# Kernel optimization log

Measured on AMD Instinct MI355X. Metric: run time of the kernel, lower is better.

## Reference

```python
import jax, jax.numpy as jnp
import numpy as np

EPS = 1e-7  # keras backend.epsilon()
NUM_ROUTING = 3


def squash(v, axis=-1):
    s2 = jnp.sum(jnp.square(v), axis=axis, keepdims=True)
    scale = s2 / (1.0 + s2) / jnp.sqrt(s2 + EPS)
    return scale * v


def setup_inputs() -> dict:
    key = jax.random.key(0)
    k1, k2 = jax.random.split(key)
    B, I, Q = 64, 2048, 16      # batch, input_num_capsule, input_dim_capsule
    J, P = 32, 32               # num_capsule, dim_capsule
    inputs = jax.random.normal(k1, (B, I, Q), dtype=jnp.float32)
    # glorot-ish scale for W: [num_capsule, input_num_capsule, dim_capsule, input_dim_capsule]
    W = jax.random.normal(k2, (J, I, P, Q), dtype=jnp.float32) * (1.0 / np.sqrt(Q))
    return {"inputs": inputs, "W": W}


def reference(inputs, W):
    # inputs_hat[b,j,i,p] = sum_q inputs[b,i,q] * W[j,i,p,q]
    hat = jnp.einsum('biq,jipq->bjip', inputs, W)
    hat_stop = jax.lax.stop_gradient(hat)
    B, J, I, P = hat.shape
    b = jnp.zeros((B, J, I), dtype=hat.dtype)
    for _ in range(NUM_ROUTING - 1):
        c = jax.nn.softmax(b, axis=1)                       # softmax over num_capsule axis
        v = squash(jnp.einsum('bji,bjip->bjp', c, hat_stop))
        b = b + jnp.einsum('bjp,bjip->bji', v, hat_stop)
    c = jax.nn.softmax(b, axis=1)
    return squash(jnp.einsum('bji,bjip->bjp', c, hat))      # [B, J, P]
```

## Files before the change

kernel.cpp:

```cpp
#include <hip/hip_runtime.h>

typedef _Float16 h8 __attribute__((ext_vector_type(8)));
typedef _Float16 h4 __attribute__((ext_vector_type(4)));
typedef float f4 __attribute__((ext_vector_type(4)));

constexpr int NB = 64;
constexpr int NI = 2048;
constexpr int NQ = 16;
constexpr int NJ = 32;
constexpr int NP = 32;
constexpr int NIP = NI / 2;
constexpr int VSZ = NB * NJ * NP;


__global__ __launch_bounds__(256)
void zero_kernel(f4* __restrict__ p)
{
    const f4 z = {0.f, 0.f, 0.f, 0.f};
    p[(size_t)blockIdx.x * 256 + threadIdx.x] = z;
}

__global__ __launch_bounds__(256)
void xpack_kernel(const float* __restrict__ X, h8* __restrict__ xp)
{
    const int ip = blockIdx.x;
    const int t = threadIdx.x;
    const int bf = t >> 6, l = t & 63;
    const int b = (l & 15) + 16 * bf;
    const int i = 2 * ip + (l >= 32 ? 1 : 0);
    const int q0 = ((l >> 4) & 1) * 8;
    const float* xs = X + ((size_t)b * NI + i) * NQ + q0;
    const float4 u = *reinterpret_cast<const float4*>(xs);
    const float4 v = *reinterpret_cast<const float4*>(xs + 4);
    h8 h;
    h[0] = (_Float16)u.x; h[1] = (_Float16)u.y; h[2] = (_Float16)u.z; h[3] = (_Float16)u.w;
    h[4] = (_Float16)v.x; h[5] = (_Float16)v.y; h[6] = (_Float16)v.z; h[7] = (_Float16)v.w;
    xp[(size_t)(ip * 4 + bf) * 64 + l] = h;
}

__device__ inline float sqscale(float s2)
{
    return s2 / ((1.f + s2) * sqrtf(s2 + 1e-7f));
}

__global__ __launch_bounds__(512)
void wacc_kernel(const float* __restrict__ Wg, const h8* __restrict__ xp,
                 h8* __restrict__ wp, float* __restrict__ ACC)
{
    const int t = threadIdx.x, wv = t >> 6, l = t & 63;
    const int j = blockIdx.x >> 4, is = blockIdx.x & 15;
    const int ioff = (l >= 32) ? 1 : 0;
    const int q0 = ((l >> 4) & 1) * 8;
    const int pbase = is * 64 + wv * 8;

    f4 D[2][4];
#pragma unroll
    for (int pf = 0; pf < 2; ++pf)
#pragma unroll
        for (int bf = 0; bf < 4; ++bf) { f4 Z = {0.f, 0.f, 0.f, 0.f}; D[pf][bf] = Z; }

    const float* wgl = Wg + ((size_t)j * NI + ioff) * (NP * NQ) + (size_t)(l & 15) * NQ + q0;

    f4 u0, u1, v0, v1;
    {
        const float* s0 = wgl + (size_t)(2 * pbase) * (NP * NQ);
        u0 = *reinterpret_cast<const f4*>(s0);
        u1 = *reinterpret_cast<const f4*>(s0 + 4);
        v0 = *reinterpret_cast<const f4*>(s0 + 16 * NQ);
        v1 = *reinterpret_cast<const f4*>(s0 + 16 * NQ + 4);
    }
    h8 B0, B1, B2, B3;
    {
        const h8* xpb = xp + (size_t)pbase * 4 * 64 + l;
        B0 = xpb[0]; B1 = xpb[64]; B2 = xpb[128]; B3 = xpb[192];
    }

#pragma unroll 1
    for (int ipl = 0; ipl < 8; ++ipl) {
        const int ipg = pbase + ipl;
        const int nip = (ipl < 7) ? ipg + 1 : ipg;
        f4 nu0, nu1, nv0, nv1;
        {
            const float* s0 = wgl + (size_t)(2 * nip) * (NP * NQ);
            nu0 = *reinterpret_cast<const f4*>(s0);
            nu1 = *reinterpret_cast<const f4*>(s0 + 4);
            nv0 = *reinterpret_cast<const f4*>(s0 + 16 * NQ);
            nv1 = *reinterpret_cast<const f4*>(s0 + 16 * NQ + 4);
        }
        h8 nB0, nB1, nB2, nB3;
        {
            const h8* xpb = xp + (size_t)nip * 4 * 64 + l;
            nB0 = xpb[0]; nB1 = xpb[64]; nB2 = xpb[128]; nB3 = xpb[192];
        }

        h8 A0, A1;
#pragma unroll
        for (int e = 0; e < 4; ++e) {
            A0[e] = (_Float16)u0[e]; A0[e + 4] = (_Float16)u1[e];
            A1[e] = (_Float16)v0[e]; A1[e + 4] = (_Float16)v1[e];
        }
        const size_t wo = ((size_t)j * NIP + ipg) * 2 * 64 + l;
        wp[wo] = A0;
        wp[wo + 64] = A1;
        D[0][0] = __builtin_amdgcn_mfma_f32_16x16x32_f16(A0, B0, D[0][0], 0, 0, 0);
        D[1][0] = __builtin_amdgcn_mfma_f32_16x16x32_f16(A1, B0, D[1][0], 0, 0, 0);
        D[0][1] = __builtin_amdgcn_mfma_f32_16x16x32_f16(A0, B1, D[0][1], 0, 0, 0);
        D[1][1] = __builtin_amdgcn_mfma_f32_16x16x32_f16(A1, B1, D[1][1], 0, 0, 0);
        D[0][2] = __builtin_amdgcn_mfma_f32_16x16x32_f16(A0, B2, D[0][2], 0, 0, 0);
        D[1][2] = __builtin_amdgcn_mfma_f32_16x16x32_f16(A1, B2, D[1][2], 0, 0, 0);
        D[0][3] = __builtin_amdgcn_mfma_f32_16x16x32_f16(A0, B3, D[0][3], 0, 0, 0);
        D[1][3] = __builtin_amdgcn_mfma_f32_16x16x32_f16(A1, B3, D[1][3], 0, 0, 0);
        u0 = nu0; u1 = nu1; v0 = nv0; v1 = nv1;
        B0 = nB0; B1 = nB1; B2 = nB2; B3 = nB3;
    }

    __shared__ float R[8][64 * 36];
#pragma unroll
    for (int pf = 0; pf < 2; ++pf)
#pragma unroll
        for (int bf = 0; bf < 4; ++bf) {
            const int b = (l & 15) + 16 * bf, p = (l >> 4) * 4 + 16 * pf;
            *reinterpret_cast<f4*>(&R[wv][b * 36 + p]) = D[pf][bf];
        }
    __syncthreads();
#pragma unroll
    for (int k = 0; k < 4; ++k) {
        const int id = t + k * 512;
        const int b = id >> 5, p = id & 31;
        float s = 0.f;
#pragma unroll
        for (int w8 = 0; w8 < 8; ++w8) s += R[w8][b * 36 + p];
        atomicAdd(ACC + ((size_t)b * NJ + j) * NP + p, s);
    }
}

__global__ __launch_bounds__(512)
void logits_kernel(const h8* __restrict__ wp, const h8* __restrict__ xp,
                   const float* __restrict__ S, _Float16* __restrict__ cp)
{
    __shared__ float L[8][32][64];
    const int t = threadIdx.x, wv = t >> 6, l = t & 63;
    const int i0 = blockIdx.x * 8;
    const int ip0 = blockIdx.x * 4;
    const bool lo = l >= 32;
    h8 zh;
#pragma unroll
    for (int e = 0; e < 8; ++e) zh[e] = (_Float16)0.f;

#pragma unroll 1
    for (int jj = 0; jj < 4; ++jj) {
        const int j = wv * 4 + jj;

        float sreg[4][8];
#pragma unroll
        for (int bf = 0; bf < 4; ++bf) {
            const int b = (l & 15) + 16 * bf;
            const size_t base = ((size_t)b * NJ + j) * NP + (l >> 4) * 4;
            const f4 s0 = *reinterpret_cast<const f4*>(S + base);
            const f4 s1 = *reinterpret_cast<const f4*>(S + base + 16);
#pragma unroll
            for (int r = 0; r < 4; ++r) { sreg[bf][r] = s0[r]; sreg[bf][4 + r] = s1[r]; }
        }

        const h8* wj = wp + (size_t)j * NIP * 2 * 64 + l;
        h8 A0 = wj[(size_t)ip0 * 128];
        h8 A1 = wj[(size_t)ip0 * 128 + 64];

#pragma unroll 1
        for (int ipl = 0; ipl < 4; ++ipl) {
            const int ipg = ip0 + ipl;
            const int nip = (ipl < 3) ? ipg + 1 : ipg;
            h8 nA0 = wj[(size_t)nip * 128];
            h8 nA1 = wj[(size_t)nip * 128 + 64];

            const h8* xpb = xp + (size_t)ipg * 4 * 64 + l;

#pragma unroll
            for (int half = 0; half < 2; ++half) {
                f4 D[2][4];
#pragma unroll
                for (int pf = 0; pf < 2; ++pf)
#pragma unroll
                    for (int bf = 0; bf < 4; ++bf) { f4 Z = {0.f, 0.f, 0.f, 0.f}; D[pf][bf] = Z; }
#pragma unroll
                for (int bfp = 0; bfp < 2; ++bfp) {
                    const h8 Ba = xpb[(2 * bfp) * 64];
                    const h8 Bb = xpb[(2 * bfp + 1) * 64];
                    const h8 Bma = ((half == 0) == lo) ? zh : Ba;
                    const h8 Bmb = ((half == 0) == lo) ? zh : Bb;
                    D[0][2 * bfp]     = __builtin_amdgcn_mfma_f32_16x16x32_f16(A0, Bma, D[0][2 * bfp], 0, 0, 0);
                    D[1][2 * bfp]     = __builtin_amdgcn_mfma_f32_16x16x32_f16(A1, Bma, D[1][2 * bfp], 0, 0, 0);
                    D[0][2 * bfp + 1] = __builtin_amdgcn_mfma_f32_16x16x32_f16(A0, Bmb, D[0][2 * bfp + 1], 0, 0, 0);
                    D[1][2 * bfp + 1] = __builtin_amdgcn_mfma_f32_16x16x32_f16(A1, Bmb, D[1][2 * bfp + 1], 0, 0, 0);
                }
                float part[4];
#pragma unroll
                for (int bf = 0; bf < 4; ++bf) {
                    float p_ = 0.f;
#pragma unroll
                    for (int pf = 0; pf < 2; ++pf)
#pragma unroll
                        for (int r = 0; r < 4; ++r) p_ += sreg[bf][pf * 4 + r] * D[pf][bf][r];
                    p_ += __shfl_xor(p_, 16);
                    p_ += __shfl_xor(p_, 32);
                    part[bf] = p_;
                }
                const int hb = l >> 4;
                const float wval = hb == 0 ? part[0] : hb == 1 ? part[1] : hb == 2 ? part[2] : part[3];
                L[ipl * 2 + half][j][(l & 15) + 16 * hb] = wval;
            }
            A0 = nA0; A1 = nA1;
        }
    }
    __syncthreads();

    {
        const int b = t & 63, ii = t >> 6;
        float lv[32];
        float m = -1e30f;
#pragma unroll
        for (int j = 0; j < 32; ++j) { lv[j] = L[ii][j][b]; m = fmaxf(m, lv[j]); }
        float s = 0.f;
#pragma unroll
        for (int j = 0; j < 32; ++j) { lv[j] = __expf(lv[j] - m); s += lv[j]; }
        const float inv = 1.f / s;
#pragma unroll
        for (int j = 0; j < 32; ++j) L[ii][j][b] = lv[j] * inv;
    }
    __syncthreads();

    {
        const int jw = t >> 4, r = t & 15;
#pragma unroll 1
        for (int ii = 0; ii < 8; ++ii) {
            h4 c4;
#pragma unroll
            for (int e = 0; e < 4; ++e) c4[e] = (_Float16)L[ii][jw][16 * e + r];
            *reinterpret_cast<h4*>(cp + ((size_t)jw * NI + i0 + ii) * 64 + r * 4) = c4;
        }
    }
}

__global__ __launch_bounds__(512)
void accum_kernel(const h8* __restrict__ wp, const h8* __restrict__ xp,
                  const _Float16* __restrict__ cp, float* __restrict__ ACC)
{
    const int t = threadIdx.x, wv = t >> 6, l = t & 63;
    const int j = blockIdx.x >> 4, is = blockIdx.x & 15;
    const int ioff = (l >= 32) ? 1 : 0;

    f4 D[2][4];
#pragma unroll
    for (int pf = 0; pf < 2; ++pf)
#pragma unroll
        for (int bf = 0; bf < 4; ++bf) { f4 Z = {0.f, 0.f, 0.f, 0.f}; D[pf][bf] = Z; }

    const int pbase = is * 64 + wv * 8;
    const h8* wj = wp + (size_t)j * NIP * 2 * 64 + l;
    const _Float16* cj = cp + ((size_t)j * NI + ioff) * 64 + (l & 15) * 4;

    h8 A0 = wj[(size_t)pbase * 128];
    h8 A1 = wj[(size_t)pbase * 128 + 64];
    h8 B0, B1, B2, B3;
    {
        const h8* xpb = xp + (size_t)pbase * 4 * 64 + l;
        B0 = xpb[0]; B1 = xpb[64]; B2 = xpb[128]; B3 = xpb[192];
    }
    h4 c4 = *reinterpret_cast<const h4*>(cj + (size_t)(2 * pbase) * 64);

#pragma unroll 1
    for (int ipl = 0; ipl < 8; ++ipl) {
        const int ipg = pbase + ipl;
        const int nip = (ipl < 7) ? ipg + 1 : ipg;
        h8 nA0 = wj[(size_t)nip * 128];
        h8 nA1 = wj[(size_t)nip * 128 + 64];
        h8 nB0, nB1, nB2, nB3;
        {
            const h8* xpb = xp + (size_t)nip * 4 * 64 + l;
            nB0 = xpb[0]; nB1 = xpb[64]; nB2 = xpb[128]; nB3 = xpb[192];
        }
        h4 nc4 = *reinterpret_cast<const h4*>(cj + (size_t)(2 * nip) * 64);

        h8 b0 = B0 * c4[0], b1 = B1 * c4[1], b2 = B2 * c4[2], b3 = B3 * c4[3];
        D[0][0] = __builtin_amdgcn_mfma_f32_16x16x32_f16(A0, b0, D[0][0], 0, 0, 0);
        D[1][0] = __builtin_amdgcn_mfma_f32_16x16x32_f16(A1, b0, D[1][0], 0, 0, 0);
        D[0][1] = __builtin_amdgcn_mfma_f32_16x16x32_f16(A0, b1, D[0][1], 0, 0, 0);
        D[1][1] = __builtin_amdgcn_mfma_f32_16x16x32_f16(A1, b1, D[1][1], 0, 0, 0);
        D[0][2] = __builtin_amdgcn_mfma_f32_16x16x32_f16(A0, b2, D[0][2], 0, 0, 0);
        D[1][2] = __builtin_amdgcn_mfma_f32_16x16x32_f16(A1, b2, D[1][2], 0, 0, 0);
        D[0][3] = __builtin_amdgcn_mfma_f32_16x16x32_f16(A0, b3, D[0][3], 0, 0, 0);
        D[1][3] = __builtin_amdgcn_mfma_f32_16x16x32_f16(A1, b3, D[1][3], 0, 0, 0);
        A0 = nA0; A1 = nA1; B0 = nB0; B1 = nB1; B2 = nB2; B3 = nB3; c4 = nc4;
    }

    __shared__ float R[8][64 * 36];
#pragma unroll
    for (int pf = 0; pf < 2; ++pf)
#pragma unroll
        for (int bf = 0; bf < 4; ++bf) {
            const int b = (l & 15) + 16 * bf, p = (l >> 4) * 4 + 16 * pf;
            *reinterpret_cast<f4*>(&R[wv][b * 36 + p]) = D[pf][bf];
        }
    __syncthreads();
#pragma unroll
    for (int k = 0; k < 4; ++k) {
        const int id = t + k * 512;
        const int b = id >> 5, p = id & 31;
        float s = 0.f;
#pragma unroll
        for (int w8 = 0; w8 < 8; ++w8) s += R[w8][b * 36 + p];
        atomicAdd(ACC + ((size_t)b * NJ + j) * NP + p, s);
    }
}

__global__ __launch_bounds__(256)
void squash_kernel(const float* __restrict__ U, const float* __restrict__ ADD,
                   float* __restrict__ OUT, float scale)
{
    const int t   = threadIdx.x;
    const int row = blockIdx.x * 8 + (t >> 5);
    const int p   = t & 31;
    const float val = U[row * 32 + p] * scale;
    float sq = val * val;
#pragma unroll
    for (int d = 1; d < 32; d <<= 1) sq += __shfl_xor(sq, d);
    float o = val * sqscale(sq);
    if (ADD != nullptr) o += ADD[row * 32 + p];
    OUT[row * 32 + p] = o;
}

extern "C" void kernel_launch(void* const* d_in, const int* in_sizes, int n_in,
                              void* d_out, int out_size, void* d_ws, size_t ws_size,
                              hipStream_t stream)
{
    const float* X  = (const float*)d_in[0];
    const float* Wg = (const float*)d_in[1];
    float* out = (float*)d_out;

    float* v1u = (float*)d_ws;
    float* v2u = v1u + VSZ;
    float* ou  = v2u + VSZ;
    float* S2  = ou  + VSZ;
    float* S3  = S2  + VSZ;
    h8* xp = (h8*)((char*)d_ws + (size_t)5 * VSZ * 4);
    _Float16* cp = (_Float16*)((char*)xp + (size_t)NIP * 4 * 64 * 16);
    h8* wpk = (h8*)((char*)cp + (size_t)NJ * NI * 64 * 2);

    xpack_kernel<<<NIP, 256, 0, stream>>>(X, xp);
    zero_kernel<<<3 * VSZ * 4 / (256 * 16), 256, 0, stream>>>((f4*)d_ws);

    wacc_kernel<<<512, 512, 0, stream>>>(Wg, xp, wpk, v1u);

    squash_kernel<<<VSZ / 256, 256, 0, stream>>>(v1u, nullptr, S2, 1.f / 32.f);
    logits_kernel<<<NI / 8, 512, 0, stream>>>(wpk, xp, S2, cp);
    accum_kernel<<<512, 512, 0, stream>>>(wpk, xp, cp, v2u);

    squash_kernel<<<VSZ / 256, 256, 0, stream>>>(v2u, S2, S3, 1.f);
    logits_kernel<<<NI / 8, 512, 0, stream>>>(wpk, xp, S3, cp);
    accum_kernel<<<512, 512, 0, stream>>>(wpk, xp, cp, ou);

    squash_kernel<<<VSZ / 256, 256, 0, stream>>>(ou, nullptr, out, 1.f);
}
```

Measured before the change: 136.5 us.

## Process two output capsules per block in accum kernel, sharing input fragments

Each block of the accumulation kernel now handles a pair of j capsules over half as many i-pairs per wave. The packed input (B) fragments are loaded once and reused across both j's. The grid keeps the same block count, and the loop count per wave drops from 8 to 4. The explicit software prefetch of the next iteration's operands is removed and replaced by straight loads, and the LDS reduction is done twice, once per j. The change cuts x-fragment traffic but costs double the accumulator registers and may expose load latency without the prefetch.

```diff
diff --git a/kernel.cpp b/kernel.cpp
--- a/kernel.cpp
+++ b/kernel.cpp
@@ -246,70 +246,81 @@
                   const _Float16* __restrict__ cp, float* __restrict__ ACC)
 {
     const int t = threadIdx.x, wv = t >> 6, l = t & 63;
-    const int j = blockIdx.x >> 4, is = blockIdx.x & 15;
+    const int jp = blockIdx.x >> 5, is = blockIdx.x & 31;
+    const int j0 = jp * 2;
     const int ioff = (l >= 32) ? 1 : 0;
 
-    f4 D[2][4];
-#pragma unroll
-    for (int pf = 0; pf < 2; ++pf)
-#pragma unroll
-        for (int bf = 0; bf < 4; ++bf) { f4 Z = {0.f, 0.f, 0.f, 0.f}; D[pf][bf] = Z; }
-
-    const int pbase = is * 64 + wv * 8;
-    const h8* wj = wp + (size_t)j * NIP * 2 * 64 + l;
-    const _Float16* cj = cp + ((size_t)j * NI + ioff) * 64 + (l & 15) * 4;
-
-    h8 A0 = wj[(size_t)pbase * 128];
-    h8 A1 = wj[(size_t)pbase * 128 + 64];
-    h8 B0, B1, B2, B3;
-    {
-        const h8* xpb = xp + (size_t)pbase * 4 * 64 + l;
-        B0 = xpb[0]; B1 = xpb[64]; B2 = xpb[128]; B3 = xpb[192];
-    }
-    h4 c4 = *reinterpret_cast<const h4*>(cj + (size_t)(2 * pbase) * 64);
-
-#pragma unroll 1
-    for (int ipl = 0; ipl < 8; ++ipl) {
+    f4 D[2][2][4];
+#pragma unroll
+    for (int jj = 0; jj < 2; ++jj)
+#pragma unroll
+        for (int pf = 0; pf < 2; ++pf)
+#pragma unroll
+            for (int bf = 0; bf < 4; ++bf) { f4 Z = {0.f, 0.f, 0.f, 0.f}; D[jj][pf][bf] = Z; }
+
+    const int pbase = is * 32 + wv * 4;
+    const h8* wj0 = wp + (size_t)j0 * NIP * 2 * 64 + l;
+    const h8* wj1 = wj0 + (size_t)NIP * 2 * 64;
+    const _Float16* cj0 = cp + ((size_t)j0 * NI + ioff) * 64 + (l & 15) * 4;
+    const _Float16* cj1 = cj0 + (size_t)NI * 64;
+
+#pragma unroll 1
+    for (int ipl = 0; ipl < 4; ++ipl) {
         const int ipg = pbase + ipl;
-        const int nip = (ipl < 7) ? ipg + 1 : ipg;
-        h8 nA0 = wj[(size_t)nip * 128];
-        h8 nA1 = wj[(size_t)nip * 128 + 64];
-        h8 nB0, nB1, nB2, nB3;
+        const h8* xpb = xp + (size_t)ipg * 4 * 64 + l;
+        const h8 B0 = xpb[0], B1 = xpb[64], B2 = xpb[128], B3 = xpb[192];
+        const h8 A00 = wj0[(size_t)ipg * 128];
+        const h8 A01 = wj0[(size_t)ipg * 128 + 64];
+        const h8 A10 = wj1[(size_t)ipg * 128];
+        const h8 A11 = wj1[(size_t)ipg * 128 + 64];
+        const h4 c0 = *reinterpret_cast<const h4*>(cj0 + (size_t)(2 * ipg) * 64);
+        const h4 c1 = *reinterpret_cast<const h4*>(cj1 + (size_t)(2 * ipg) * 64);
+
         {
-            const h8* xpb = xp + (size_t)nip * 4 * 64 + l;
-            nB0 = xpb[0]; nB1 = xpb[64]; nB2 = xpb[128]; nB3 = xpb[192];
-        }
-        h4 nc4 = *reinterpret_cast<const h4*>(cj + (size_t)(2 * nip) * 64);
-
-        h8 b0 = B0 * c4[0], b1 = B1 * c4[1], b2 = B2 * c4[2], b3 = B3 * c4[3];
-        D[0][0] = __builtin_amdgcn_mfma_f32_16x16x32_f16(A0, b0, D[0][0], 0, 0, 0);
-        D[1][0] = __builtin_amdgcn_mfma_f32_16x16x32_f16(A1, b0, D[1][0], 0, 0, 0);
-        D[0][1] = __builtin_amdgcn_mfma_f32_16x16x32_f16(A0, b1, D[0][1], 0, 0, 0);
-        D[1][1] = __builtin_amdgcn_mfma_f32_16x16x32_f16(A1, b1, D[1][1], 0, 0, 0);
-        D[0][2] = __builtin_amdgcn_mfma_f32_16x16x32_f16(A0, b2, D[0][2], 0, 0, 0);
-        D[1][2] = __builtin_amdgcn_mfma_f32_16x16x32_f16(A1, b2, D[1][2], 0, 0, 0);
-        D[0][3] = __builtin_amdgcn_mfma_f32_16x16x32_f16(A0, b3, D[0][3], 0, 0, 0);
-        D[1][3] = __builtin_amdgcn_mfma_f32_16x16x32_f16(A1, b3, D[1][3], 0, 0, 0);
-        A0 = nA0; A1 = nA1; B0 = nB0; B1 = nB1; B2 = nB2; B3 = nB3; c4 = nc4;
+            const h8 b0 = B0 * c0[0], b1 = B1 * c0[1], b2 = B2 * c0[2], b3 = B3 * c0[3];
+            D[0][0][0] = __builtin_amdgcn_mfma_f32_16x16x32_f16(A00, b0, D[0][0][0], 0, 0, 0);
+            D[0][1][0] = __builtin_amdgcn_mfma_f32_16x16x32_f16(A01, b0, D[0][1][0], 0, 0, 0);
+            D[0][0][1] = __builtin_amdgcn_mfma_f32_16x16x32_f16(A00, b1, D[0][0][1], 0, 0, 0);
+            D[0][1][1] = __builtin_amdgcn_mfma_f32_16x16x32_f16(A01, b1, D[0][1][1], 0, 0, 0);
+            D[0][0][2] = __builtin_amdgcn_mfma_f32_16x16x32_f16(A00, b2, D[0][0][2], 0, 0, 0);
+            D[0][1][2] = __builtin_amdgcn_mfma_f32_16x16x32_f16(A01, b2, D[0][1][2], 0, 0, 0);
+            D[0][0][3] = __builtin_amdgcn_mfma_f32_16x16x32_f16(A00, b3, D[0][0][3], 0, 0, 0);
+            D[0][1][3] = __builtin_amdgcn_mfma_f32_16x16x32_f16(A01, b3, D[0][1][3], 0, 0, 0);
+        }
+        {
+            const h8 b0 = B0 * c1[0], b1 = B1 * c1[1], b2 = B2 * c1[2], b3 = B3 * c1[3];
+            D[1][0][0] = __builtin_amdgcn_mfma_f32_16x16x32_f16(A10, b0, D[1][0][0], 0, 0, 0);
+            D[1][1][0] = __builtin_amdgcn_mfma_f32_16x16x32_f16(A11, b0, D[1][1][0], 0, 0, 0);
+            D[1][0][1] = __builtin_amdgcn_mfma_f32_16x16x32_f16(A10, b1, D[1][0][1], 0, 0, 0);
+            D[1][1][1] = __builtin_amdgcn_mfma_f32_16x16x32_f16(A11, b1, D[1][1][1], 0, 0, 0);
+            D[1][0][2] = __builtin_amdgcn_mfma_f32_16x16x32_f16(A10, b2, D[1][0][2], 0, 0, 0);
+            D[1][1][2] = __builtin_amdgcn_mfma_f32_16x16x32_f16(A11, b2, D[1][1][2], 0, 0, 0);
+            D[1][0][3] = __builtin_amdgcn_mfma_f32_16x16x32_f16(A10, b3, D[1][0][3], 0, 0, 0);
+            D[1][1][3] = __builtin_amdgcn_mfma_f32_16x16x32_f16(A11, b3, D[1][1][3], 0, 0, 0);
+        }
     }
 
     __shared__ float R[8][64 * 36];
-#pragma unroll
-    for (int pf = 0; pf < 2; ++pf)
-#pragma unroll
-        for (int bf = 0; bf < 4; ++bf) {
-            const int b = (l & 15) + 16 * bf, p = (l >> 4) * 4 + 16 * pf;
-            *reinterpret_cast<f4*>(&R[wv][b * 36 + p]) = D[pf][bf];
-        }
-    __syncthreads();
-#pragma unroll
-    for (int k = 0; k < 4; ++k) {
-        const int id = t + k * 512;
-        const int b = id >> 5, p = id & 31;
-        float s = 0.f;
-#pragma unroll
-        for (int w8 = 0; w8 < 8; ++w8) s += R[w8][b * 36 + p];
-        atomicAdd(ACC + ((size_t)b * NJ + j) * NP + p, s);
+#pragma unroll 1
+    for (int jj = 0; jj < 2; ++jj) {
+        if (jj) __syncthreads();
+#pragma unroll
+        for (int pf = 0; pf < 2; ++pf)
+#pragma unroll
+            for (int bf = 0; bf < 4; ++bf) {
+                const int b = (l & 15) + 16 * bf, p = (l >> 4) * 4 + 16 * pf;
+                *reinterpret_cast<f4*>(&R[wv][b * 36 + p]) = D[jj][pf][bf];
+            }
+        __syncthreads();
+#pragma unroll
+        for (int k = 0; k < 4; ++k) {
+            const int id = t + k * 512;
+            const int b = id >> 5, p = id & 31;
+            float s = 0.f;
+#pragma unroll
+            for (int w8 = 0; w8 < 8; ++w8) s += R[w8][b * 36 + p];
+            atomicAdd(ACC + ((size_t)b * NJ + (j0 + jj)) * NP + p, s);
+        }
     }
 }
 
```

Result: slower. 185.6 us (+36.0%).
